# Kernel optimization log

Measured on AMD Instinct MI355X. Metric: run time of the kernel, lower is better.

## Reference

```python
import jax, jax.numpy as jnp
import numpy as np

NUM_HEADS = 8
NUM_GROUPS = 32
EPS = 1e-5

def group_norm(x, w, b):
    B, C, H, W = x.shape
    xg = x.reshape(B, NUM_GROUPS, -1)
    mean = xg.mean(axis=-1, keepdims=True)
    var = xg.var(axis=-1, keepdims=True)
    xg = (xg - mean) * jax.lax.rsqrt(var + EPS)
    return xg.reshape(B, C, H, W) * w[None, :, None, None] + b[None, :, None, None]

def setup_inputs() -> dict:
    key = jax.random.key(0)
    ks = jax.random.split(key, 3)
    B, C, H, W = 16, 512, 32, 32
    x = jax.random.normal(ks[0], (B, C, H, W), dtype=jnp.float32)
    norm_w = jnp.ones((C,), jnp.float32)
    norm_b = jnp.zeros((C,), jnp.float32)
    qkv_w = jax.random.normal(ks[1], (3 * C, C), dtype=jnp.float32) * (C ** -0.5)
    qkv_b = jnp.zeros((3 * C,), jnp.float32)
    proj_w = jax.random.normal(ks[2], (C, C), dtype=jnp.float32) * (C ** -0.5)
    proj_b = jnp.zeros((C,), jnp.float32)
    return {"x": x, "norm_w": norm_w, "norm_b": norm_b, "qkv_w": qkv_w,
            "qkv_b": qkv_b, "proj_w": proj_w, "proj_b": proj_b}

def reference(x, norm_w, norm_b, qkv_w, qkv_b, proj_w, proj_b):
    B, C, H, W = x.shape
    nh, hd = NUM_HEADS, C // NUM_HEADS
    L = H * W
    h = group_norm(x, norm_w, norm_b)
    # 1x1 conv == channel matmul
    qkv = jnp.einsum('oc,bcl->bol', qkv_w, h.reshape(B, C, L)) + qkv_b[None, :, None]
    qkv = qkv.reshape(B, 3, nh, hd, L)
    qkv = jnp.transpose(qkv, (1, 0, 2, 4, 3))  # (3, B, nh, L, hd)
    q, k, v = qkv[0], qkv[1], qkv[2]
    scale = hd ** -0.5
    attn = jax.nn.softmax(jnp.einsum('bnqd,bnkd->bnqk', q, k) * scale, axis=-1)
    h = jnp.einsum('bnqk,bnkd->bnqd', attn, v)          # (B, nh, L, hd)
    h = jnp.transpose(h, (0, 1, 3, 2)).reshape(B, C, L)  # (B, C, L)
    h = jnp.einsum('oc,bcl->bol', proj_w, h) + proj_b[None, :, None]
    return h.reshape(B, C, H, W) + x
```

## Files before the change

kernel.cpp:

```cpp
#include <hip/hip_runtime.h>

#define BATCH 16
#define CCH   512
#define LSEQ  1024
#define NH    8
#define HD    64
#define NG    32
#define CPG   16
#define EPS   1e-5f

typedef __attribute__((ext_vector_type(8))) short short8;
typedef __attribute__((ext_vector_type(4))) float f32x4;
#define MFMA __builtin_amdgcn_mfma_f32_16x16x32_bf16

__device__ inline short f2bf(float f) {
  unsigned u = __float_as_uint(f);
  u += 0x7FFFu + ((u >> 16) & 1u);
  return (short)(u >> 16);
}

__global__ __launch_bounds__(256) void cvt_kernel(const float* __restrict__ src,
                                                  short* __restrict__ dst) {
  const int i = blockIdx.x * 256 + threadIdx.x;
  const float4 v = ((const float4*)src)[i];
  short vals[4] = {f2bf(v.x), f2bf(v.y), f2bf(v.z), f2bf(v.w)};
  *(uint2*)(dst + (size_t)i * 4) = *(uint2*)vals;
}

__global__ __launch_bounds__(256) void gn_kernel(
    const float* __restrict__ x, const float* __restrict__ nw,
    const float* __restrict__ nb, short* __restrict__ hT)
{
  const int g = blockIdx.x, b = blockIdx.y;
  const size_t base = ((size_t)b * CCH + (size_t)g * CPG) * LSEQ;
  const float4* __restrict__ x4 = (const float4*)(x + base);
  const int tid = threadIdx.x;

  __shared__ short T[16][1026];
  __shared__ float red0[4], red1[4];

  float4 v[16];
  float s = 0.f, s2 = 0.f;
#pragma unroll
  for (int r = 0; r < 16; ++r) {
    v[r] = x4[tid + 256 * r];
    s  += (v[r].x + v[r].y) + (v[r].z + v[r].w);
    s2 += (v[r].x * v[r].x + v[r].y * v[r].y) + (v[r].z * v[r].z + v[r].w * v[r].w);
  }
#pragma unroll
  for (int m = 1; m < 64; m <<= 1) { s += __shfl_xor(s, m); s2 += __shfl_xor(s2, m); }
  const int wid = tid >> 6;
  if ((tid & 63) == 0) { red0[wid] = s; red1[wid] = s2; }
  __syncthreads();
  const float ts  = (red0[0] + red0[1]) + (red0[2] + red0[3]);
  const float ts2 = (red1[0] + red1[1]) + (red1[2] + red1[3]);
  const float mean = ts * (1.f / 16384.f);
  const float var  = ts2 * (1.f / 16384.f) - mean * mean;
  const float rstd = rsqrtf(var + EPS);
#pragma unroll
  for (int r = 0; r < 16; ++r) {
    const int e = tid + 256 * r;
    const int c = e >> 8, l4 = (e & 255) * 4;
    const float sc = rstd * nw[g * CPG + c];
    const float sh = nb[g * CPG + c] - mean * sc;
    T[c][l4 + 0] = f2bf(v[r].x * sc + sh);
    T[c][l4 + 1] = f2bf(v[r].y * sc + sh);
    T[c][l4 + 2] = f2bf(v[r].z * sc + sh);
    T[c][l4 + 3] = f2bf(v[r].w * sc + sh);
  }
  __syncthreads();
  short* __restrict__ outp = hT + (size_t)b * LSEQ * CCH + g * CPG;
#pragma unroll
  for (int it = 0; it < 4; ++it) {
    const int l = tid + 256 * it;
    short vals[16];
#pragma unroll
    for (int c = 0; c < 16; ++c) vals[c] = T[c][l];
    *(short8*)(outp + (size_t)l * CCH)     = *(short8*)&vals[0];
    *(short8*)(outp + (size_t)l * CCH + 8) = *(short8*)&vals[8];
  }
}

__global__ __launch_bounds__(256) void qkv_gemm(
    const short* __restrict__ Wb, const float* __restrict__ bias,
    const short* __restrict__ hT, short* __restrict__ qT,
    short* __restrict__ kT, short* __restrict__ vv)
{
  const int b = blockIdx.z, my = blockIdx.y;
  const int m0 = my * 128, n0 = blockIdx.x * 128;
  const short* __restrict__ Bsrc = hT + (size_t)b * LSEQ * CCH;

  __shared__ short smem[2 * 128 * 72];
  short (*As)[72] = (short (*)[72])smem;
  short (*Bs)[72] = (short (*)[72])(smem + 128 * 72);

  const int tid = threadIdx.x, lane = tid & 63, w = tid >> 6;
  const int wm = (w >> 1) * 64, wn = (w & 1) * 64;
  const int l15 = lane & 15, l4g = lane >> 4;
  const int srow = tid >> 3, sk8 = (tid & 7) * 8;

  const f32x4 fz = {0.f, 0.f, 0.f, 0.f};
  f32x4 acc[4][4];
#pragma unroll
  for (int i = 0; i < 4; ++i)
#pragma unroll
    for (int j = 0; j < 4; ++j) acc[i][j] = fz;

  for (int k0 = 0; k0 < CCH; k0 += 64) {
    __syncthreads();
#pragma unroll
    for (int it = 0; it < 4; ++it) {
      const int row = srow + it * 32;
      *(short8*)&As[row][sk8] = *(const short8*)(Wb + (size_t)(m0 + row) * CCH + k0 + sk8);
      *(short8*)&Bs[row][sk8] = *(const short8*)(Bsrc + (size_t)(n0 + row) * CCH + k0 + sk8);
    }
    __syncthreads();
#pragma unroll
    for (int kk = 0; kk < 2; ++kk) {
      const int ko = kk * 32 + l4g * 8;
      short8 af[4], bf[4];
#pragma unroll
      for (int i = 0; i < 4; ++i) af[i] = *(const short8*)&As[wm + i * 16 + l15][ko];
#pragma unroll
      for (int j = 0; j < 4; ++j) bf[j] = *(const short8*)&Bs[wn + j * 16 + l15][ko];
#pragma unroll
      for (int i = 0; i < 4; ++i)
#pragma unroll
        for (int j = 0; j < 4; ++j)
          acc[i][j] = MFMA(af[i], bf[j], acc[i][j], 0, 0, 0);
    }
  }

  const int region = my >> 2;
  const float scale = (region == 0) ? 0.125f : 1.0f;
  short (*CT)[136] = (short (*)[136])smem;

  __syncthreads();
#pragma unroll
  for (int i = 0; i < 4; ++i)
#pragma unroll
    for (int r = 0; r < 4; ++r) {
      const int cl = wm + i * 16 + l4g * 4 + r;
      const float bb = bias[m0 + cl];
#pragma unroll
      for (int j = 0; j < 4; ++j) {
        const int ll = wn + j * 16 + l15;
        const short bv = f2bf((acc[i][j][r] + bb) * scale);
        if (region == 2) CT[cl][ll] = bv; else CT[ll][cl] = bv;
      }
    }
  __syncthreads();
#pragma unroll
  for (int it = 0; it < 8; ++it) {
    const int f = tid + it * 256;
    const int rr = f >> 4, c8 = (f & 15) * 8;
    const short8 val = *(const short8*)&CT[rr][c8];
    if (region == 2) {
      *(short8*)(vv + (size_t)b * CCH * LSEQ + (size_t)((my & 3) * 128 + rr) * LSEQ + n0 + c8) = val;
    } else {
      short* __restrict__ dst = (region == 0) ? qT : kT;
      *(short8*)(dst + (size_t)b * LSEQ * CCH + (size_t)(n0 + rr) * CCH + (my & 3) * 128 + c8) = val;
    }
  }
}

__global__ __launch_bounds__(256) void attn_kernel(
    const short* __restrict__ qT, const short* __restrict__ kT,
    const short* __restrict__ vv, short* __restrict__ oT)
{
  const int qt = blockIdx.x, hh = blockIdx.y, b = blockIdx.z;
  const int l0 = qt * 64, h64 = hh * 64;
  const int tid = threadIdx.x, lane = tid & 63, w = tid >> 6;
  const int l15 = lane & 15, l4g = lane >> 4;
  const int wq = w * 16;

  __shared__ short Ks[64][72];
  __shared__ short Vs[64][72];
  __shared__ unsigned Pw[4][16][36];

  const short* __restrict__ qb = qT + (size_t)b * LSEQ * CCH;
  const short* __restrict__ kb = kT + (size_t)b * LSEQ * CCH;
  const short* __restrict__ vb = vv + (size_t)b * CCH * LSEQ;

  short8 qf[2];
#pragma unroll
  for (int kk = 0; kk < 2; ++kk)
    qf[kk] = *(const short8*)(qb + (size_t)(l0 + wq + l15) * CCH + h64 + kk * 32 + l4g * 8);

  const f32x4 fz = {0.f, 0.f, 0.f, 0.f};
  f32x4 o[4];
#pragma unroll
  for (int df = 0; df < 4; ++df) o[df] = fz;
  float mr = -1.0e30f, lr = 0.f;

  const int srow = tid >> 3, sk8 = (tid & 7) * 8;

  for (int jt = 0; jt < 16; ++jt) {
    const int j0 = jt * 64;
    __syncthreads();
#pragma unroll
    for (int it = 0; it < 2; ++it) {
      const int row = srow + it * 32;
      *(short8*)&Ks[row][sk8] = *(const short8*)(kb + (size_t)(j0 + row) * CCH + h64 + sk8);
      *(short8*)&Vs[row][sk8] = *(const short8*)(vb + (size_t)(h64 + row) * LSEQ + j0 + sk8);
    }
    __syncthreads();

    f32x4 s[4];
#pragma unroll
    for (int j = 0; j < 4; ++j) s[j] = fz;
#pragma unroll
    for (int kk = 0; kk < 2; ++kk) {
      const int ko = kk * 32 + l4g * 8;
      short8 kf[4];
#pragma unroll
      for (int j = 0; j < 4; ++j) kf[j] = *(const short8*)&Ks[j * 16 + l15][ko];
#pragma unroll
      for (int j = 0; j < 4; ++j) s[j] = MFMA(kf[j], qf[kk], s[j], 0, 0, 0);
    }

    float mx = s[0][0];
#pragma unroll
    for (int j = 0; j < 4; ++j)
#pragma unroll
      for (int r = 0; r < 4; ++r) mx = fmaxf(mx, s[j][r]);
    mx = fmaxf(mx, __shfl_xor(mx, 16));
    mx = fmaxf(mx, __shfl_xor(mx, 32));
    const float mnew = fmaxf(mr, mx);
    const float corr = __expf(mr - mnew);
    mr = mnew;

    float rs = 0.f;
    unsigned pk[4][2];
#pragma unroll
    for (int j = 0; j < 4; ++j) {
      float p0 = __expf(s[j][0] - mnew), p1 = __expf(s[j][1] - mnew);
      float p2 = __expf(s[j][2] - mnew), p3 = __expf(s[j][3] - mnew);
      rs += (p0 + p1) + (p2 + p3);
      pk[j][0] = (unsigned)(unsigned short)f2bf(p0) | ((unsigned)(unsigned short)f2bf(p1) << 16);
      pk[j][1] = (unsigned)(unsigned short)f2bf(p2) | ((unsigned)(unsigned short)f2bf(p3) << 16);
    }
    rs += __shfl_xor(rs, 16);
    rs += __shfl_xor(rs, 32);
    lr = lr * corr + rs;

#pragma unroll
    for (int j = 0; j < 4; ++j)
      *(uint2*)&Pw[w][l15][j * 8 + l4g * 2] = make_uint2(pk[j][0], pk[j][1]);

    float cb[4];
#pragma unroll
    for (int r = 0; r < 4; ++r) cb[r] = __shfl(corr, l4g * 4 + r);
#pragma unroll
    for (int df = 0; df < 4; ++df)
#pragma unroll
      for (int r = 0; r < 4; ++r) o[df][r] *= cb[r];

#pragma unroll
    for (int kk = 0; kk < 2; ++kk) {
      const short8 pf = *(const short8*)&Pw[w][l15][kk * 16 + l4g * 4];
      const int ko = kk * 32 + l4g * 8;
#pragma unroll
      for (int df = 0; df < 4; ++df) {
        const short8 vf = *(const short8*)&Vs[df * 16 + l15][ko];
        o[df] = MFMA(pf, vf, o[df], 0, 0, 0);
      }
    }
  }

  float lb[4];
#pragma unroll
  for (int r = 0; r < 4; ++r) lb[r] = 1.f / __shfl(lr, l4g * 4 + r);
  short* __restrict__ ob = oT + (size_t)b * LSEQ * CCH;
#pragma unroll
  for (int df = 0; df < 4; ++df)
#pragma unroll
    for (int r = 0; r < 4; ++r)
      ob[(size_t)(l0 + wq + l4g * 4 + r) * CCH + h64 + df * 16 + l15] = f2bf(o[df][r] * lb[r]);
}

__global__ __launch_bounds__(256) void proj_gemm(
    const short* __restrict__ Wb, const float* __restrict__ bias,
    const short* __restrict__ oT, const float* __restrict__ x,
    float* __restrict__ out)
{
  const int b = blockIdx.z;
  const int m0 = blockIdx.y * 128, n0 = blockIdx.x * 128;
  const short* __restrict__ Bsrc = oT + (size_t)b * LSEQ * CCH;

  __shared__ short As[128][72];
  __shared__ short Bs[128][72];

  const int tid = threadIdx.x, lane = tid & 63, w = tid >> 6;
  const int wm = (w >> 1) * 64, wn = (w & 1) * 64;
  const int l15 = lane & 15, l4g = lane >> 4;
  const int srow = tid >> 3, sk8 = (tid & 7) * 8;

  const f32x4 fz = {0.f, 0.f, 0.f, 0.f};
  f32x4 acc[4][4];
#pragma unroll
  for (int i = 0; i < 4; ++i)
#pragma unroll
    for (int j = 0; j < 4; ++j) acc[i][j] = fz;

  for (int k0 = 0; k0 < CCH; k0 += 64) {
    __syncthreads();
#pragma unroll
    for (int it = 0; it < 4; ++it) {
      const int row = srow + it * 32;
      *(short8*)&As[row][sk8] = *(const short8*)(Wb + (size_t)(m0 + row) * CCH + k0 + sk8);
      *(short8*)&Bs[row][sk8] = *(const short8*)(Bsrc + (size_t)(n0 + row) * CCH + k0 + sk8);
    }
    __syncthreads();
#pragma unroll
    for (int kk = 0; kk < 2; ++kk) {
      const int ko = kk * 32 + l4g * 8;
      short8 af[4], bf[4];
#pragma unroll
      for (int i = 0; i < 4; ++i) af[i] = *(const short8*)&As[wm + i * 16 + l15][ko];
#pragma unroll
      for (int j = 0; j < 4; ++j) bf[j] = *(const short8*)&Bs[wn + j * 16 + l15][ko];
#pragma unroll
      for (int i = 0; i < 4; ++i)
#pragma unroll
        for (int j = 0; j < 4; ++j)
          acc[i][j] = MFMA(af[i], bf[j], acc[i][j], 0, 0, 0);
    }
  }

  const size_t obase = (size_t)b * CCH * LSEQ;
#pragma unroll
  for (int i = 0; i < 4; ++i)
#pragma unroll
    for (int r = 0; r < 4; ++r) {
      const int gm = m0 + wm + i * 16 + l4g * 4 + r;
      const float bb = bias[gm];
#pragma unroll
      for (int j = 0; j < 4; ++j) {
        const int gl = n0 + wn + j * 16 + l15;
        const size_t idx = obase + (size_t)gm * LSEQ + gl;
        out[idx] = acc[i][j][r] + bb + x[idx];
      }
    }
}

extern "C" void kernel_launch(void* const* d_in, const int* in_sizes, int n_in,
                              void* d_out, int out_size, void* d_ws, size_t ws_size,
                              hipStream_t stream)
{
  const float* x      = (const float*)d_in[0];
  const float* norm_w = (const float*)d_in[1];
  const float* norm_b = (const float*)d_in[2];
  const float* qkv_w  = (const float*)d_in[3];
  const float* qkv_b  = (const float*)d_in[4];
  const float* proj_w = (const float*)d_in[5];
  const float* proj_b = (const float*)d_in[6];
  float* out = (float*)d_out;

  char* ws = (char*)d_ws;
  short* wq16 = (short*)ws;
  short* wp16 = (short*)(ws + 1572864);
  short* hT   = (short*)(ws + 2097152);
  short* qT   = (short*)(ws + 2097152 + 16777216);
  short* kT   = (short*)(ws + 2097152 + 2 * 16777216);
  short* vv   = (short*)(ws + 2097152 + 3 * 16777216);
  short* oT   = (short*)(ws + 2097152 + 4 * 16777216);

  cvt_kernel<<<768, 256, 0, stream>>>(qkv_w, wq16);
  cvt_kernel<<<256, 256, 0, stream>>>(proj_w, wp16);
  gn_kernel<<<dim3(NG, BATCH), 256, 0, stream>>>(x, norm_w, norm_b, hT);
  qkv_gemm<<<dim3(8, 12, BATCH), 256, 0, stream>>>(wq16, qkv_b, hT, qT, kT, vv);
  attn_kernel<<<dim3(16, NH, BATCH), 256, 0, stream>>>(qT, kT, vv, oT);
  proj_gemm<<<dim3(8, 4, BATCH), 256, 0, stream>>>(wp16, proj_b, oT, x, out);
}
```

Measured before the change: 260.9 us.

## Double-buffer GEMM and attention tiles with direct global-to-LDS loads and XOR swizzle

Replaces the register-staged shared-memory tile loads in the QKV GEMM, attention, and projection GEMM kernels with global_load_lds direct transfers into double-buffered LDS. The next tile is fetched while the current one is consumed, and each iteration needs one barrier instead of two. The padded layout is replaced by an XOR swizzle to avoid bank conflicts. The softmax bf16 packing also switches to the library float2-to-bf16 intrinsic. LDS use doubles, which may lower occupancy, and the swizzled layout and vmcnt waits must line up exactly for results to stay correct.

```diff
diff --git a/kernel.cpp b/kernel.cpp
--- a/kernel.cpp
+++ b/kernel.cpp
@@ -1,4 +1,5 @@
 #include <hip/hip_runtime.h>
+#include <hip/hip_bf16.h>
 
 #define BATCH 16
 #define CCH   512
@@ -18,6 +19,13 @@
   u += 0x7FFFu + ((u >> 16) & 1u);
   return (short)(u >> 16);
 }
+
+__device__ inline void gl2lds16(const short* g, short* l) {
+  __builtin_amdgcn_global_load_lds(
+      (const __attribute__((address_space(1))) unsigned*)g,
+      (__attribute__((address_space(3))) unsigned*)l, 16, 0, 0);
+}
+#define VMCNT0() asm volatile("s_waitcnt vmcnt(0)" ::: "memory")
 
 __global__ __launch_bounds__(256) void cvt_kernel(const float* __restrict__ src,
                                                   short* __restrict__ dst) {
@@ -90,14 +98,12 @@
   const int m0 = my * 128, n0 = blockIdx.x * 128;
   const short* __restrict__ Bsrc = hT + (size_t)b * LSEQ * CCH;
 
-  __shared__ short smem[2 * 128 * 72];
-  short (*As)[72] = (short (*)[72])smem;
-  short (*Bs)[72] = (short (*)[72])(smem + 128 * 72);
-
+  __shared__ short smem[32768];
   const int tid = threadIdx.x, lane = tid & 63, w = tid >> 6;
   const int wm = (w >> 1) * 64, wn = (w & 1) * 64;
   const int l15 = lane & 15, l4g = lane >> 4;
-  const int srow = tid >> 3, sk8 = (tid & 7) * 8;
+  const int sr = lane >> 3, c8 = ((lane & 7) ^ (lane >> 3)) * 8;
+  const int swz = (l15 & 7) << 4;
 
   const f32x4 fz = {0.f, 0.f, 0.f, 0.f};
   f32x4 acc[4][4];
@@ -106,36 +112,50 @@
 #pragma unroll
     for (int j = 0; j < 4; ++j) acc[i][j] = fz;
 
-  for (int k0 = 0; k0 < CCH; k0 += 64) {
-    __syncthreads();
-#pragma unroll
-    for (int it = 0; it < 4; ++it) {
-      const int row = srow + it * 32;
-      *(short8*)&As[row][sk8] = *(const short8*)(Wb + (size_t)(m0 + row) * CCH + k0 + sk8);
-      *(short8*)&Bs[row][sk8] = *(const short8*)(Bsrc + (size_t)(n0 + row) * CCH + k0 + sk8);
-    }
-    __syncthreads();
+#define QSTAGE(ks, bb)                                                        \
+  {                                                                           \
+    const int k0_ = (ks) * 64;                                                \
+    _Pragma("unroll")                                                         \
+    for (int i_ = 0; i_ < 4; ++i_) {                                          \
+      const int rb_ = w * 32 + i_ * 8;                                        \
+      gl2lds16(Wb   + (size_t)(m0 + rb_ + sr) * CCH + k0_ + c8,               \
+               &smem[(bb) * 8192 + rb_ * 64]);                                \
+      gl2lds16(Bsrc + (size_t)(n0 + rb_ + sr) * CCH + k0_ + c8,               \
+               &smem[16384 + (bb) * 8192 + rb_ * 64]);                        \
+    }                                                                         \
+  }
+
+  QSTAGE(0, 0);
+  VMCNT0();
+  __syncthreads();
+
+  for (int ks = 0; ks < 8; ++ks) {
+    const int bb = ks & 1;
+    if (ks < 7) QSTAGE(ks + 1, bb ^ 1);
 #pragma unroll
     for (int kk = 0; kk < 2; ++kk) {
-      const int ko = kk * 32 + l4g * 8;
+      const int ko = (kk * 64 + l4g * 16) ^ swz;
       short8 af[4], bf[4];
 #pragma unroll
-      for (int i = 0; i < 4; ++i) af[i] = *(const short8*)&As[wm + i * 16 + l15][ko];
-#pragma unroll
-      for (int j = 0; j < 4; ++j) bf[j] = *(const short8*)&Bs[wn + j * 16 + l15][ko];
+      for (int i = 0; i < 4; ++i)
+        af[i] = *(const short8*)((const char*)&smem[bb * 8192 + (wm + i * 16 + l15) * 64] + ko);
+#pragma unroll
+      for (int j = 0; j < 4; ++j)
+        bf[j] = *(const short8*)((const char*)&smem[16384 + bb * 8192 + (wn + j * 16 + l15) * 64] + ko);
 #pragma unroll
       for (int i = 0; i < 4; ++i)
 #pragma unroll
         for (int j = 0; j < 4; ++j)
           acc[i][j] = MFMA(af[i], bf[j], acc[i][j], 0, 0, 0);
     }
+    VMCNT0();
+    __syncthreads();
   }
 
   const int region = my >> 2;
   const float scale = (region == 0) ? 0.125f : 1.0f;
   short (*CT)[136] = (short (*)[136])smem;
 
-  __syncthreads();
 #pragma unroll
   for (int i = 0; i < 4; ++i)
 #pragma unroll
@@ -153,13 +173,13 @@
 #pragma unroll
   for (int it = 0; it < 8; ++it) {
     const int f = tid + it * 256;
-    const int rr = f >> 4, c8 = (f & 15) * 8;
-    const short8 val = *(const short8*)&CT[rr][c8];
+    const int rr = f >> 4, cc8 = (f & 15) * 8;
+    const short8 val = *(const short8*)&CT[rr][cc8];
     if (region == 2) {
-      *(short8*)(vv + (size_t)b * CCH * LSEQ + (size_t)((my & 3) * 128 + rr) * LSEQ + n0 + c8) = val;
+      *(short8*)(vv + (size_t)b * CCH * LSEQ + (size_t)((my & 3) * 128 + rr) * LSEQ + n0 + cc8) = val;
     } else {
       short* __restrict__ dst = (region == 0) ? qT : kT;
-      *(short8*)(dst + (size_t)b * LSEQ * CCH + (size_t)(n0 + rr) * CCH + (my & 3) * 128 + c8) = val;
+      *(short8*)(dst + (size_t)b * LSEQ * CCH + (size_t)(n0 + rr) * CCH + (my & 3) * 128 + cc8) = val;
     }
   }
 }
@@ -174,8 +194,8 @@
   const int l15 = lane & 15, l4g = lane >> 4;
   const int wq = w * 16;
 
-  __shared__ short Ks[64][72];
-  __shared__ short Vs[64][72];
+  __shared__ short Ks[2][64][64];
+  __shared__ short Vs[2][64][64];
   __shared__ unsigned Pw[4][16][36];
 
   const short* __restrict__ qb = qT + (size_t)b * LSEQ * CCH;
@@ -193,28 +213,40 @@
   for (int df = 0; df < 4; ++df) o[df] = fz;
   float mr = -1.0e30f, lr = 0.f;
 
-  const int srow = tid >> 3, sk8 = (tid & 7) * 8;
+  const int sr = lane >> 3, c8 = ((lane & 7) ^ (lane >> 3)) * 8;
+  const int swz = (l15 & 7) << 4;
+
+#define ASTAGE(jt_, bb)                                                       \
+  {                                                                           \
+    const int j0_ = (jt_) * 64;                                               \
+    _Pragma("unroll")                                                         \
+    for (int i_ = 0; i_ < 2; ++i_) {                                          \
+      const int rb_ = w * 16 + i_ * 8;                                        \
+      gl2lds16(kb + (size_t)(j0_ + rb_ + sr) * CCH + h64 + c8,                \
+               &Ks[bb][rb_][0]);                                              \
+      gl2lds16(vb + (size_t)(h64 + rb_ + sr) * LSEQ + j0_ + c8,               \
+               &Vs[bb][rb_][0]);                                              \
+    }                                                                         \
+  }
+
+  ASTAGE(0, 0);
+  VMCNT0();
+  __syncthreads();
 
   for (int jt = 0; jt < 16; ++jt) {
-    const int j0 = jt * 64;
-    __syncthreads();
-#pragma unroll
-    for (int it = 0; it < 2; ++it) {
-      const int row = srow + it * 32;
-      *(short8*)&Ks[row][sk8] = *(const short8*)(kb + (size_t)(j0 + row) * CCH + h64 + sk8);
-      *(short8*)&Vs[row][sk8] = *(const short8*)(vb + (size_t)(h64 + row) * LSEQ + j0 + sk8);
-    }
-    __syncthreads();
+    const int bb = jt & 1;
+    if (jt < 15) ASTAGE(jt + 1, bb ^ 1);
 
     f32x4 s[4];
 #pragma unroll
     for (int j = 0; j < 4; ++j) s[j] = fz;
 #pragma unroll
     for (int kk = 0; kk < 2; ++kk) {
-      const int ko = kk * 32 + l4g * 8;
+      const int ko = (kk * 64 + l4g * 16) ^ swz;
       short8 kf[4];
 #pragma unroll
-      for (int j = 0; j < 4; ++j) kf[j] = *(const short8*)&Ks[j * 16 + l15][ko];
+      for (int j = 0; j < 4; ++j)
+        kf[j] = *(const short8*)((const char*)&Ks[bb][j * 16 + l15][0] + ko);
 #pragma unroll
       for (int j = 0; j < 4; ++j) s[j] = MFMA(kf[j], qf[kk], s[j], 0, 0, 0);
     }
@@ -237,8 +269,10 @@
       float p0 = __expf(s[j][0] - mnew), p1 = __expf(s[j][1] - mnew);
       float p2 = __expf(s[j][2] - mnew), p3 = __expf(s[j][3] - mnew);
       rs += (p0 + p1) + (p2 + p3);
-      pk[j][0] = (unsigned)(unsigned short)f2bf(p0) | ((unsigned)(unsigned short)f2bf(p1) << 16);
-      pk[j][1] = (unsigned)(unsigned short)f2bf(p2) | ((unsigned)(unsigned short)f2bf(p3) << 16);
+      __hip_bfloat162 w0 = __float22bfloat162_rn(make_float2(p0, p1));
+      __hip_bfloat162 w1 = __float22bfloat162_rn(make_float2(p2, p3));
+      pk[j][0] = *(unsigned*)&w0;
+      pk[j][1] = *(unsigned*)&w1;
     }
     rs += __shfl_xor(rs, 16);
     rs += __shfl_xor(rs, 32);
@@ -259,13 +293,15 @@
 #pragma unroll
     for (int kk = 0; kk < 2; ++kk) {
       const short8 pf = *(const short8*)&Pw[w][l15][kk * 16 + l4g * 4];
-      const int ko = kk * 32 + l4g * 8;
+      const int ko = (kk * 64 + l4g * 16) ^ swz;
 #pragma unroll
       for (int df = 0; df < 4; ++df) {
-        const short8 vf = *(const short8*)&Vs[df * 16 + l15][ko];
+        const short8 vf = *(const short8*)((const char*)&Vs[bb][df * 16 + l15][0] + ko);
         o[df] = MFMA(pf, vf, o[df], 0, 0, 0);
       }
     }
+    VMCNT0();
+    __syncthreads();
   }
 
   float lb[4];
@@ -288,13 +324,12 @@
   const int m0 = blockIdx.y * 128, n0 = blockIdx.x * 128;
   const short* __restrict__ Bsrc = oT + (size_t)b * LSEQ * CCH;
 
-  __shared__ short As[128][72];
-  __shared__ short Bs[128][72];
-
+  __shared__ short smem[32768];
   const int tid = threadIdx.x, lane = tid & 63, w = tid >> 6;
   const int wm = (w >> 1) * 64, wn = (w & 1) * 64;
   const int l15 = lane & 15, l4g = lane >> 4;
-  const int srow = tid >> 3, sk8 = (tid & 7) * 8;
+  const int sr = lane >> 3, c8 = ((lane & 7) ^ (lane >> 3)) * 8;
+  const int swz = (l15 & 7) << 4;
 
   const f32x4 fz = {0.f, 0.f, 0.f, 0.f};
   f32x4 acc[4][4];
@@ -303,29 +338,44 @@
 #pragma unroll
     for (int j = 0; j < 4; ++j) acc[i][j] = fz;
 
-  for (int k0 = 0; k0 < CCH; k0 += 64) {
-    __syncthreads();
-#pragma unroll
-    for (int it = 0; it < 4; ++it) {
-      const int row = srow + it * 32;
-      *(short8*)&As[row][sk8] = *(const short8*)(Wb + (size_t)(m0 + row) * CCH + k0 + sk8);
-      *(short8*)&Bs[row][sk8] = *(const short8*)(Bsrc + (size_t)(n0 + row) * CCH + k0 + sk8);
-    }
-    __syncthreads();
+#define PSTAGE(ks, bb)                                                        \
+  {                                                                           \
+    const int k0_ = (ks) * 64;                                                \
+    _Pragma("unroll")                                                         \
+    for (int i_ = 0; i_ < 4; ++i_) {                                          \
+      const int rb_ = w * 32 + i_ * 8;                                        \
+      gl2lds16(Wb   + (size_t)(m0 + rb_ + sr) * CCH + k0_ + c8,               \
+               &smem[(bb) * 8192 + rb_ * 64]);                                \
+      gl2lds16(Bsrc + (size_t)(n0 + rb_ + sr) * CCH + k0_ + c8,               \
+               &smem[16384 + (bb) * 8192 + rb_ * 64]);                        \
+    }                                                                         \
+  }
+
+  PSTAGE(0, 0);
+  VMCNT0();
+  __syncthreads();
+
+  for (int ks = 0; ks < 8; ++ks) {
+    const int bb = ks & 1;
+    if (ks < 7) PSTAGE(ks + 1, bb ^ 1);
 #pragma unroll
     for (int kk = 0; kk < 2; ++kk) {
-      const int ko = kk * 32 + l4g * 8;
+      const int ko = (kk * 64 + l4g * 16) ^ swz;
       short8 af[4], bf[4];
 #pragma unroll
-      for (int i = 0; i < 4; ++i) af[i] = *(const short8*)&As[wm + i * 16 + l15][ko];
-#pragma unroll
-      for (int j = 0; j < 4; ++j) bf[j] = *(const short8*)&Bs[wn + j * 16 + l15][ko];
+      for (int i = 0; i < 4; ++i)
+        af[i] = *(const short8*)((const char*)&smem[bb * 8192 + (wm + i * 16 + l15) * 64] + ko);
+#pragma unroll
+      for (int j = 0; j < 4; ++j)
+        bf[j] = *(const short8*)((const char*)&smem[16384 + bb * 8192 + (wn + j * 16 + l15) * 64] + ko);
 #pragma unroll
       for (int i = 0; i < 4; ++i)
 #pragma unroll
         for (int j = 0; j < 4; ++j)
           acc[i][j] = MFMA(af[i], bf[j], acc[i][j], 0, 0, 0);
     }
+    VMCNT0();
+    __syncthreads();
   }
 
   const size_t obase = (size_t)b * CCH * LSEQ;
```

New measurement: 243.1 us. 6.8% less time.
